# Kernel tuning notes

Measured on AMD Instinct MI355X. Metric: run time of the kernel, lower is better.

## Reference

```python
import jax, jax.numpy as jnp
import numpy as np
import math

B, S, IN, H, M = 4, 2048, 256, 128, 128  # mem_dim must equal hidden_size


def _xavier(key, shape):
    fan_in, fan_out = shape[0], shape[-1]
    lim = math.sqrt(6.0 / (fan_in + fan_out))
    return jax.random.uniform(key, shape, jnp.float32, -lim, lim)


def setup_inputs() -> dict:
    key = jax.random.key(0)
    ks = jax.random.split(key, 8)
    return dict(
        x=jax.random.normal(ks[0], (B, S, IN), jnp.float32),
        c0=jnp.zeros((M, M), jnp.float32),   # init_hidden matrix memory
        n0=jnp.zeros((M, 1), jnp.float32),   # init_hidden normalizer
        w_q=_xavier(ks[1], (IN, H)), b_q=jnp.zeros((H,), jnp.float32),
        w_k=_xavier(ks[2], (IN, M)), b_k=jnp.zeros((M,), jnp.float32),
        w_v=_xavier(ks[3], (IN, M)), b_v=jnp.zeros((M,), jnp.float32),
        w_i=_xavier(ks[4], (IN, 1)), b_i=jnp.zeros((1,), jnp.float32),
        w_f=_xavier(ks[5], (IN, 1)), b_f=jnp.zeros((1,), jnp.float32),
        w_o=_xavier(ks[6], (IN, H)), b_o=jnp.zeros((H,), jnp.float32),
    )


def reference(x, c0, n0, w_q, b_q, w_k, b_k, w_v, b_v, w_i, b_i, w_f, b_f, w_o, b_o):
    Bb, Ss, Ii = x.shape
    Mm = w_k.shape[1]
    Hh = w_q.shape[1]
    xf = x.reshape(Bb * Ss, Ii)                                  # [N, IN]
    q = xf @ w_q + b_q                                           # [N, H]
    k = (xf @ w_k + b_k) * (1.0 / math.sqrt(Mm))                 # [N, M]
    v = xf @ w_v + b_v                                           # [N, M]
    i_t = jnp.exp(xf @ w_i + b_i)                                # [N, 1]
    f_t = jax.nn.sigmoid(xf @ w_f + b_f)                         # [N, 1]
    # Original loop never updates c_prev: c_t[n] = f[n]*c0 + i[n]*outer(v[n], k[n])
    c = f_t[:, :, None] * c0[None] + i_t[:, :, None] * (v[:, :, None] * k[:, None, :])  # [N, M, M]
    n = f_t[:, :, None] * n0[None] + i_t[:, :, None] * k[:, :, None]                    # [N, M, 1]
    c = c.reshape(Bb, Ss, Mm, Mm)
    n = n.reshape(Bb, Ss, Mm, 1)
    q4 = q.reshape(Bb, Ss, Hh)
    nq = jnp.einsum('bsm,bsm->bs', n[..., 0], q4)                # n^T q
    denom = jnp.maximum(jnp.abs(nq), 1.0)[..., None]             # max(|n^T q|, 1)
    h_tilde = jnp.einsum('bsmk,bsk->bsm', c, q4) / denom         # (c_t q) / denom
    o = jax.nn.sigmoid(xf @ w_o + b_o).reshape(Bb, Ss, Hh)
    h = o * h_tilde                                              # [B, S, H]
    return (h, c, n)
```

## Files before the change

kernel.cpp:

```cpp
#include <hip/hip_runtime.h>
#include <math.h>

#define B_    4
#define S_    2048
#define IN_   256
#define H_    128
#define M_    128
#define NROWS (B_ * S_)
#define RPB   16
#define GRP   4
#define TPB   256
#define XPAD  260

typedef float f4_t __attribute__((ext_vector_type(4)));

__global__ __launch_bounds__(TPB) void xlstm_fused(
    const float* __restrict__ x,
    const float* __restrict__ c0,
    const float* __restrict__ n0,
    const float* __restrict__ w_q, const float* __restrict__ b_q,
    const float* __restrict__ w_k, const float* __restrict__ b_k,
    const float* __restrict__ w_v, const float* __restrict__ b_v,
    const float* __restrict__ w_i, const float* __restrict__ b_i,
    const float* __restrict__ w_f, const float* __restrict__ b_f,
    const float* __restrict__ w_o, const float* __restrict__ b_o,
    float* __restrict__ out_h,
    float* __restrict__ out_c,
    float* __restrict__ out_n)
{
    __shared__ float xs[RPB][XPAD];
    __shared__ float qs[RPB][M_];
    __shared__ float ks[RPB][M_];
    __shared__ float vs[RPB][M_];
    __shared__ float os_[RPB][M_];
    __shared__ float itf[RPB][2];
    __shared__ float scal[RPB][2];

    const int t    = threadIdx.x;
    const int row0 = blockIdx.x * RPB;

    for (int p4 = t; p4 < RPB * IN_ / 4; p4 += TPB) {
        int p = p4 * 4;
        float4 v = *(const float4*)(x + (size_t)row0 * IN_ + p);
        int r = p >> 8, c = p & 255;
        *(float4*)&xs[r][c] = v;
    }
    __syncthreads();

    {
        const int gr = t >> 4, gseg = t & 15;
        const float* xrow = &xs[gr][gseg * 16];
        float pi = 0.f, pf = 0.f;
        #pragma unroll
        for (int u = 0; u < 4; ++u) {
            float4 xv  = *(const float4*)(xrow + u * 4);
            float4 wiv = *(const float4*)(w_i + gseg * 16 + u * 4);
            float4 wfv = *(const float4*)(w_f + gseg * 16 + u * 4);
            pi = fmaf(xv.x, wiv.x, fmaf(xv.y, wiv.y, fmaf(xv.z, wiv.z, fmaf(xv.w, wiv.w, pi))));
            pf = fmaf(xv.x, wfv.x, fmaf(xv.y, wfv.y, fmaf(xv.z, wfv.z, fmaf(xv.w, wfv.w, pf))));
        }
        #pragma unroll
        for (int m = 1; m < 16; m <<= 1) { pi += __shfl_xor(pi, m); pf += __shfl_xor(pf, m); }
        if (gseg == 0) {
            itf[gr][0] = __expf(pi + b_i[0]);
            itf[gr][1] = 1.f / (1.f + __expf(-(pf + b_f[0])));
        }
    }

    const int cg  = t & 31;
    const int mat = (t >> 5) & 3;
    const int rh  = t >> 7;
    const int c4  = cg * 4;

    const float* W    = (mat == 0) ? w_q : (mat == 1) ? w_k : (mat == 2) ? w_v : w_o;
    const float* BIAS = (mat == 0) ? b_q : (mat == 1) ? b_k : (mat == 2) ? b_v : b_o;
    float (*DST)[M_]  = (mat == 0) ? qs  : (mat == 1) ? ks  : (mat == 2) ? vs  : os_;
    const f4_t b4 = *(const f4_t*)(BIAS + c4);
    const float kscale = 0.08838834764831843f;

    const int col = t & 127;

    #pragma unroll 1
    for (int g = 0; g < 4; ++g) {
        const int r0 = g * GRP + rh * 2;

        f4_t acc0 = (f4_t){0.f,0.f,0.f,0.f};
        f4_t acc1 = (f4_t){0.f,0.f,0.f,0.f};
        #pragma unroll 4
        for (int it = 0; it < 64; ++it) {
            const int k0 = it * 4;
            const float* wp = W + (size_t)k0 * H_ + c4;
            f4_t w0 = *(const f4_t*)(wp);
            f4_t w1 = *(const f4_t*)(wp + H_);
            f4_t w2 = *(const f4_t*)(wp + 2 * H_);
            f4_t w3 = *(const f4_t*)(wp + 3 * H_);
            f4_t xv0 = *(const f4_t*)&xs[r0][k0];
            f4_t xv1 = *(const f4_t*)&xs[r0 + 1][k0];
            acc0 += xv0.x * w0 + xv0.y * w1 + xv0.z * w2 + xv0.w * w3;
            acc1 += xv1.x * w0 + xv1.y * w1 + xv1.z * w2 + xv1.w * w3;
        }
        acc0 += b4; acc1 += b4;
        if (mat == 1) { acc0 *= kscale; acc1 *= kscale; }
        if (mat == 3) {
            acc0.x = 1.f/(1.f+__expf(-acc0.x)); acc0.y = 1.f/(1.f+__expf(-acc0.y));
            acc0.z = 1.f/(1.f+__expf(-acc0.z)); acc0.w = 1.f/(1.f+__expf(-acc0.w));
            acc1.x = 1.f/(1.f+__expf(-acc1.x)); acc1.y = 1.f/(1.f+__expf(-acc1.y));
            acc1.z = 1.f/(1.f+__expf(-acc1.z)); acc1.w = 1.f/(1.f+__expf(-acc1.w));
        }
        *(f4_t*)&DST[r0][c4]     = acc0;
        *(f4_t*)&DST[r0 + 1][c4] = acc1;
        __syncthreads();

        float c0q0 = 0.f, c0q1 = 0.f;
        {
            const float* c0row = c0 + (size_t)col * M_;
            #pragma unroll 2
            for (int j4 = 0; j4 < M_; j4 += 4) {
                f4_t w4 = *(const f4_t*)(c0row + j4);
                f4_t qa = *(const f4_t*)&qs[r0][j4];
                f4_t qb = *(const f4_t*)&qs[r0 + 1][j4];
                c0q0 = fmaf(w4.x, qa.x, fmaf(w4.y, qa.y, fmaf(w4.z, qa.z, fmaf(w4.w, qa.w, c0q0))));
                c0q1 = fmaf(w4.x, qb.x, fmaf(w4.y, qb.y, fmaf(w4.z, qb.z, fmaf(w4.w, qb.w, c0q1))));
            }
        }

        {
            const int srow = g * GRP + (t >> 6);
            const int l    = t & 63;
            float ka = ks[srow][l],      kb = ks[srow][l + 64];
            float qa = qs[srow][l],      qb = qs[srow][l + 64];
            float na = n0[l],            nb = n0[l + 64];
            float pkq = fmaf(ka, qa, kb * qb);
            float pnq = fmaf(na, qa, nb * qb);
            #pragma unroll
            for (int m = 1; m < 64; m <<= 1) { pkq += __shfl_xor(pkq, m); pnq += __shfl_xor(pnq, m); }
            if (l == 0) { scal[srow][0] = pkq; scal[srow][1] = pnq; }
        }
        __syncthreads();

        #pragma unroll
        for (int rr = 0; rr < 2; ++rr) {
            const int row = r0 + rr;
            const size_t grow = (size_t)(row0 + row);
            const float iv = itf[row][0], fv = itf[row][1];
            const float kv = ks[row][col];
            out_n[grow * M_ + col] = fmaf(fv, n0[col], iv * kv);
            const float nq    = fmaf(fv, scal[row][1], iv * scal[row][0]);
            const float denom = fmaxf(fabsf(nq), 1.0f);
            const float c0q   = rr ? c0q1 : c0q0;
            const float ht = fmaf(fv, c0q, iv * vs[row][col] * scal[row][0]) / denom;
            out_h[grow * H_ + col] = os_[row][col] * ht;
        }

        {
            const int base = t * 4;
            const int j    = base & 127;
            #pragma unroll 2
            for (int ch = 0; ch < 16; ++ch) {
                const int p = (ch << 10) + base;
                const int m = p >> 7;
                f4_t c0v = *(const f4_t*)(c0 + p);
                #pragma unroll
                for (int r = 0; r < GRP; ++r) {
                    const int row = g * GRP + r;
                    f4_t k4 = *(const f4_t*)&ks[row][j];
                    float s = itf[row][0] * vs[row][m];
                    f4_t o4 = itf[row][1] * c0v + s * k4;
                    __builtin_nontemporal_store(o4,
                        (f4_t*)(out_c + (size_t)(row0 + row) * (M_ * M_) + p));
                }
            }
        }
    }
}

extern "C" void kernel_launch(void* const* d_in, const int* in_sizes, int n_in,
                              void* d_out, int out_size, void* d_ws, size_t ws_size,
                              hipStream_t stream) {
    const float* x   = (const float*)d_in[0];
    const float* c0  = (const float*)d_in[1];
    const float* n0  = (const float*)d_in[2];
    const float* w_q = (const float*)d_in[3];  const float* b_q = (const float*)d_in[4];
    const float* w_k = (const float*)d_in[5];  const float* b_k = (const float*)d_in[6];
    const float* w_v = (const float*)d_in[7];  const float* b_v = (const float*)d_in[8];
    const float* w_i = (const float*)d_in[9];  const float* b_i = (const float*)d_in[10];
    const float* w_f = (const float*)d_in[11]; const float* b_f = (const float*)d_in[12];
    const float* w_o = (const float*)d_in[13]; const float* b_o = (const float*)d_in[14];

    float* out   = (float*)d_out;
    float* out_h = out;
    float* out_c = out + (size_t)NROWS * H_;
    float* out_n = out_c + (size_t)NROWS * M_ * M_;

    hipLaunchKernelGGL(xlstm_fused, dim3(NROWS / RPB), dim3(TPB), 0, stream,
                       x, c0, n0, w_q, b_q, w_k, b_k, w_v, b_v,
                       w_i, b_i, w_f, b_f, w_o, b_o,
                       out_h, out_c, out_n);
}
```

Baseline: 147.7 us.

## Warp-specialize fused xLSTM kernel into producer and store-consumer pipeline

Doubles the block to 512 threads and splits it by role. The first 256 threads compute the q/k/v/o projections, gates, reductions and h/n outputs for one row group. The other 256 threads stream the large c outer-product stores for the previous group, with q/k/v/o held in double-buffered shared memory. The aim is to overlap the memory-bound 8192x128x128 c writes with the projection math. In exchange, each block holds more threads and registers, which lowers occupancy, and two barriers per stage can stall whichever role runs longer.

```diff
diff --git a/kernel.cpp b/kernel.cpp
--- a/kernel.cpp
+++ b/kernel.cpp
@@ -9,12 +9,13 @@
 #define NROWS (B_ * S_)
 #define RPB   16
 #define GRP   4
-#define TPB   256
+#define NGRP  4
+#define TPB   512
 #define XPAD  260
 
 typedef float f4_t __attribute__((ext_vector_type(4)));
 
-__global__ __launch_bounds__(TPB) void xlstm_fused(
+__global__ __launch_bounds__(TPB) void xlstm_pipe(
     const float* __restrict__ x,
     const float* __restrict__ c0,
     const float* __restrict__ n0,
@@ -29,148 +30,178 @@
     float* __restrict__ out_n)
 {
     __shared__ float xs[RPB][XPAD];
-    __shared__ float qs[RPB][M_];
-    __shared__ float ks[RPB][M_];
-    __shared__ float vs[RPB][M_];
-    __shared__ float os_[RPB][M_];
+    __shared__ float bq[2][GRP][M_];
+    __shared__ float bk[2][GRP][M_];
+    __shared__ float bv[2][GRP][M_];
+    __shared__ float bo[2][GRP][M_];
     __shared__ float itf[RPB][2];
-    __shared__ float scal[RPB][2];
+    __shared__ float scalb[2][GRP][2];
 
     const int t    = threadIdx.x;
     const int row0 = blockIdx.x * RPB;
+    const bool prod = (t < 256);
 
     for (int p4 = t; p4 < RPB * IN_ / 4; p4 += TPB) {
         int p = p4 * 4;
         float4 v = *(const float4*)(x + (size_t)row0 * IN_ + p);
-        int r = p >> 8, c = p & 255;
-        *(float4*)&xs[r][c] = v;
+        *(float4*)&xs[p >> 8][p & 255] = v;
     }
     __syncthreads();
 
-    {
-        const int gr = t >> 4, gseg = t & 15;
-        const float* xrow = &xs[gr][gseg * 16];
-        float pi = 0.f, pf = 0.f;
-        #pragma unroll
-        for (int u = 0; u < 4; ++u) {
-            float4 xv  = *(const float4*)(xrow + u * 4);
-            float4 wiv = *(const float4*)(w_i + gseg * 16 + u * 4);
-            float4 wfv = *(const float4*)(w_f + gseg * 16 + u * 4);
-            pi = fmaf(xv.x, wiv.x, fmaf(xv.y, wiv.y, fmaf(xv.z, wiv.z, fmaf(xv.w, wiv.w, pi))));
-            pf = fmaf(xv.x, wfv.x, fmaf(xv.y, wfv.y, fmaf(xv.z, wfv.z, fmaf(xv.w, wfv.w, pf))));
-        }
-        #pragma unroll
-        for (int m = 1; m < 16; m <<= 1) { pi += __shfl_xor(pi, m); pf += __shfl_xor(pf, m); }
-        if (gseg == 0) {
-            itf[gr][0] = __expf(pi + b_i[0]);
-            itf[gr][1] = 1.f / (1.f + __expf(-(pf + b_f[0])));
-        }
-    }
-
     const int cg  = t & 31;
     const int mat = (t >> 5) & 3;
-    const int rh  = t >> 7;
+    const int rh  = (t >> 7) & 1;
     const int c4  = cg * 4;
-
-    const float* W    = (mat == 0) ? w_q : (mat == 1) ? w_k : (mat == 2) ? w_v : w_o;
-    const float* BIAS = (mat == 0) ? b_q : (mat == 1) ? b_k : (mat == 2) ? b_v : b_o;
-    float (*DST)[M_]  = (mat == 0) ? qs  : (mat == 1) ? ks  : (mat == 2) ? vs  : os_;
-    const f4_t b4 = *(const f4_t*)(BIAS + c4);
+    const int col = t & 127;
+    const float* W    = (mat==0)? w_q : (mat==1)? w_k : (mat==2)? w_v : w_o;
+    const float* BIAS = (mat==0)? b_q : (mat==1)? b_k : (mat==2)? b_v : b_o;
+    const f4_t bias4 = *(const f4_t*)(BIAS + c4);
     const float kscale = 0.08838834764831843f;
 
-    const int col = t & 127;
+    const int ct = t & 255;
+
+    float c0qA = 0.f, c0qB = 0.f;
 
     #pragma unroll 1
-    for (int g = 0; g < 4; ++g) {
-        const int r0 = g * GRP + rh * 2;
-
-        f4_t acc0 = (f4_t){0.f,0.f,0.f,0.f};
-        f4_t acc1 = (f4_t){0.f,0.f,0.f,0.f};
-        #pragma unroll 4
-        for (int it = 0; it < 64; ++it) {
-            const int k0 = it * 4;
-            const float* wp = W + (size_t)k0 * H_ + c4;
-            f4_t w0 = *(const f4_t*)(wp);
-            f4_t w1 = *(const f4_t*)(wp + H_);
-            f4_t w2 = *(const f4_t*)(wp + 2 * H_);
-            f4_t w3 = *(const f4_t*)(wp + 3 * H_);
-            f4_t xv0 = *(const f4_t*)&xs[r0][k0];
-            f4_t xv1 = *(const f4_t*)&xs[r0 + 1][k0];
-            acc0 += xv0.x * w0 + xv0.y * w1 + xv0.z * w2 + xv0.w * w3;
-            acc1 += xv1.x * w0 + xv1.y * w1 + xv1.z * w2 + xv1.w * w3;
-        }
-        acc0 += b4; acc1 += b4;
-        if (mat == 1) { acc0 *= kscale; acc1 *= kscale; }
-        if (mat == 3) {
-            acc0.x = 1.f/(1.f+__expf(-acc0.x)); acc0.y = 1.f/(1.f+__expf(-acc0.y));
-            acc0.z = 1.f/(1.f+__expf(-acc0.z)); acc0.w = 1.f/(1.f+__expf(-acc0.w));
-            acc1.x = 1.f/(1.f+__expf(-acc1.x)); acc1.y = 1.f/(1.f+__expf(-acc1.y));
-            acc1.z = 1.f/(1.f+__expf(-acc1.z)); acc1.w = 1.f/(1.f+__expf(-acc1.w));
-        }
-        *(f4_t*)&DST[r0][c4]     = acc0;
-        *(f4_t*)&DST[r0 + 1][c4] = acc1;
-        __syncthreads();
-
-        float c0q0 = 0.f, c0q1 = 0.f;
-        {
-            const float* c0row = c0 + (size_t)col * M_;
-            #pragma unroll 2
-            for (int j4 = 0; j4 < M_; j4 += 4) {
-                f4_t w4 = *(const f4_t*)(c0row + j4);
-                f4_t qa = *(const f4_t*)&qs[r0][j4];
-                f4_t qb = *(const f4_t*)&qs[r0 + 1][j4];
-                c0q0 = fmaf(w4.x, qa.x, fmaf(w4.y, qa.y, fmaf(w4.z, qa.z, fmaf(w4.w, qa.w, c0q0))));
-                c0q1 = fmaf(w4.x, qb.x, fmaf(w4.y, qb.y, fmaf(w4.z, qb.z, fmaf(w4.w, qb.w, c0q1))));
-            }
-        }
-
-        {
-            const int srow = g * GRP + (t >> 6);
-            const int l    = t & 63;
-            float ka = ks[srow][l],      kb = ks[srow][l + 64];
-            float qa = qs[srow][l],      qb = qs[srow][l + 64];
-            float na = n0[l],            nb = n0[l + 64];
-            float pkq = fmaf(ka, qa, kb * qb);
-            float pnq = fmaf(na, qa, nb * qb);
-            #pragma unroll
-            for (int m = 1; m < 64; m <<= 1) { pkq += __shfl_xor(pkq, m); pnq += __shfl_xor(pnq, m); }
-            if (l == 0) { scal[srow][0] = pkq; scal[srow][1] = pnq; }
-        }
-        __syncthreads();
-
-        #pragma unroll
-        for (int rr = 0; rr < 2; ++rr) {
-            const int row = r0 + rr;
-            const size_t grow = (size_t)(row0 + row);
-            const float iv = itf[row][0], fv = itf[row][1];
-            const float kv = ks[row][col];
-            out_n[grow * M_ + col] = fmaf(fv, n0[col], iv * kv);
-            const float nq    = fmaf(fv, scal[row][1], iv * scal[row][0]);
-            const float denom = fmaxf(fabsf(nq), 1.0f);
-            const float c0q   = rr ? c0q1 : c0q0;
-            const float ht = fmaf(fv, c0q, iv * vs[row][col] * scal[row][0]) / denom;
-            out_h[grow * H_ + col] = os_[row][col] * ht;
-        }
-
-        {
-            const int base = t * 4;
-            const int j    = base & 127;
+    for (int s = 0; s <= NGRP; ++s) {
+        if (prod) {
+            if (s == 0) {
+                const int gr = t >> 4, gseg = t & 15;
+                const float* xrow = &xs[gr][gseg * 16];
+                float pi = 0.f, pf = 0.f;
+                #pragma unroll
+                for (int u = 0; u < 4; ++u) {
+                    float4 xv  = *(const float4*)(xrow + u * 4);
+                    float4 wiv = *(const float4*)(w_i + gseg * 16 + u * 4);
+                    float4 wfv = *(const float4*)(w_f + gseg * 16 + u * 4);
+                    pi = fmaf(xv.x,wiv.x, fmaf(xv.y,wiv.y, fmaf(xv.z,wiv.z, fmaf(xv.w,wiv.w, pi))));
+                    pf = fmaf(xv.x,wfv.x, fmaf(xv.y,wfv.y, fmaf(xv.z,wfv.z, fmaf(xv.w,wfv.w, pf))));
+                }
+                #pragma unroll
+                for (int mm = 1; mm < 16; mm <<= 1) { pi += __shfl_xor(pi, mm); pf += __shfl_xor(pf, mm); }
+                if (gseg == 0) {
+                    itf[gr][0] = __expf(pi + b_i[0]);
+                    itf[gr][1] = 1.f / (1.f + __expf(-(pf + b_f[0])));
+                }
+            }
+            if (s > 0) {
+                const int b = (s - 1) & 1;
+                #pragma unroll
+                for (int rr = 0; rr < 2; ++rr) {
+                    const int lrow = rh * 2 + rr;
+                    const int row  = (s - 1) * GRP + lrow;
+                    const size_t grow = (size_t)(row0 + row);
+                    const float iv = itf[row][0], fv = itf[row][1];
+                    out_n[grow * M_ + col] = fmaf(fv, n0[col], iv * bk[b][lrow][col]);
+                    const float kq  = scalb[b][lrow][0];
+                    const float n0q = scalb[b][lrow][1];
+                    const float nq = fmaf(fv, n0q, iv * kq);
+                    const float denom = fmaxf(fabsf(nq), 1.f);
+                    const float c0q = rr ? c0qB : c0qA;
+                    const float ht = fmaf(fv, c0q, iv * bv[b][lrow][col] * kq) / denom;
+                    out_h[grow * H_ + col] = bo[b][lrow][col] * ht;
+                }
+            }
+            if (s < NGRP) {
+                const int b  = s & 1;
+                const int r0 = s * GRP + rh * 2;
+                f4_t acc0 = (f4_t){0.f,0.f,0.f,0.f};
+                f4_t acc1 = (f4_t){0.f,0.f,0.f,0.f};
+                #pragma unroll 4
+                for (int it = 0; it < 64; ++it) {
+                    const int k0 = it * 4;
+                    const float* wp = W + (size_t)k0 * H_ + c4;
+                    f4_t w0 = *(const f4_t*)(wp);
+                    f4_t w1 = *(const f4_t*)(wp + H_);
+                    f4_t w2 = *(const f4_t*)(wp + 2 * H_);
+                    f4_t w3 = *(const f4_t*)(wp + 3 * H_);
+                    f4_t xv0 = *(const f4_t*)&xs[r0][k0];
+                    f4_t xv1 = *(const f4_t*)&xs[r0 + 1][k0];
+                    acc0 += xv0.x*w0 + xv0.y*w1 + xv0.z*w2 + xv0.w*w3;
+                    acc1 += xv1.x*w0 + xv1.y*w1 + xv1.z*w2 + xv1.w*w3;
+                }
+                acc0 += bias4; acc1 += bias4;
+                if (mat == 1) { acc0 *= kscale; acc1 *= kscale; }
+                if (mat == 3) {
+                    acc0.x = 1.f/(1.f+__expf(-acc0.x)); acc0.y = 1.f/(1.f+__expf(-acc0.y));
+                    acc0.z = 1.f/(1.f+__expf(-acc0.z)); acc0.w = 1.f/(1.f+__expf(-acc0.w));
+                    acc1.x = 1.f/(1.f+__expf(-acc1.x)); acc1.y = 1.f/(1.f+__expf(-acc1.y));
+                    acc1.z = 1.f/(1.f+__expf(-acc1.z)); acc1.w = 1.f/(1.f+__expf(-acc1.w));
+                }
+                float (*DST)[M_] = (mat==0)? bq[b] : (mat==1)? bk[b] : (mat==2)? bv[b] : bo[b];
+                const int lr = rh * 2;
+                *(f4_t*)&DST[lr][c4]     = acc0;
+                *(f4_t*)&DST[lr + 1][c4] = acc1;
+            }
+        } else if (s > 0) {
+            const int b     = (s - 1) & 1;
+            const int gbase = (s - 1) * GRP;
+            const int base  = ct * 4;
+            const int j     = base & 127;
             #pragma unroll 2
             for (int ch = 0; ch < 16; ++ch) {
                 const int p = (ch << 10) + base;
                 const int m = p >> 7;
                 f4_t c0v = *(const f4_t*)(c0 + p);
                 #pragma unroll
-                for (int r = 0; r < GRP; ++r) {
-                    const int row = g * GRP + r;
-                    f4_t k4 = *(const f4_t*)&ks[row][j];
-                    float s = itf[row][0] * vs[row][m];
-                    f4_t o4 = itf[row][1] * c0v + s * k4;
+                for (int r = 0; r < 2; ++r) {
+                    const int row = gbase + r;
+                    f4_t k4 = *(const f4_t*)&bk[b][r][j];
+                    float sf = itf[row][0] * bv[b][r][m];
+                    f4_t o4 = itf[row][1] * c0v + sf * k4;
                     __builtin_nontemporal_store(o4,
                         (f4_t*)(out_c + (size_t)(row0 + row) * (M_ * M_) + p));
                 }
             }
         }
+        __syncthreads();
+        if (prod) {
+            if (s < NGRP) {
+                const int b  = s & 1;
+                const int lr = rh * 2;
+                float a0 = 0.f, a1 = 0.f;
+                const float* c0row = c0 + (size_t)col * M_;
+                #pragma unroll 2
+                for (int j4 = 0; j4 < M_; j4 += 4) {
+                    f4_t w4 = *(const f4_t*)(c0row + j4);
+                    f4_t qa = *(const f4_t*)&bq[b][lr][j4];
+                    f4_t qb = *(const f4_t*)&bq[b][lr + 1][j4];
+                    a0 = fmaf(w4.x,qa.x, fmaf(w4.y,qa.y, fmaf(w4.z,qa.z, fmaf(w4.w,qa.w, a0))));
+                    a1 = fmaf(w4.x,qb.x, fmaf(w4.y,qb.y, fmaf(w4.z,qb.z, fmaf(w4.w,qb.w, a1))));
+                }
+                c0qA = a0; c0qB = a1;
+                const int wv = t >> 6;
+                const int l  = t & 63;
+                const float ka  = bk[b][wv][l], kb2 = bk[b][wv][l + 64];
+                const float qa2 = bq[b][wv][l], qb2 = bq[b][wv][l + 64];
+                float pkq = fmaf(ka, qa2, kb2 * qb2);
+                float pnq = fmaf(n0[l], qa2, n0[l + 64] * qb2);
+                #pragma unroll
+                for (int mm = 1; mm < 64; mm <<= 1) { pkq += __shfl_xor(pkq, mm); pnq += __shfl_xor(pnq, mm); }
+                if (l == 0) { scalb[b][wv][0] = pkq; scalb[b][wv][1] = pnq; }
+            }
+        } else if (s > 0) {
+            const int b     = (s - 1) & 1;
+            const int gbase = (s - 1) * GRP;
+            const int base  = ct * 4;
+            const int j     = base & 127;
+            #pragma unroll 2
+            for (int ch = 0; ch < 16; ++ch) {
+                const int p = (ch << 10) + base;
+                const int m = p >> 7;
+                f4_t c0v = *(const f4_t*)(c0 + p);
+                #pragma unroll
+                for (int r = 2; r < 4; ++r) {
+                    const int row = gbase + r;
+                    f4_t k4 = *(const f4_t*)&bk[b][r][j];
+                    float sf = itf[row][0] * bv[b][r][m];
+                    f4_t o4 = itf[row][1] * c0v + sf * k4;
+                    __builtin_nontemporal_store(o4,
+                        (f4_t*)(out_c + (size_t)(row0 + row) * (M_ * M_) + p));
+                }
+            }
+        }
+        __syncthreads();
     }
 }
 
@@ -192,7 +223,7 @@
     float* out_c = out + (size_t)NROWS * H_;
     float* out_n = out_c + (size_t)NROWS * M_ * M_;
 
-    hipLaunchKernelGGL(xlstm_fused, dim3(NROWS / RPB), dim3(TPB), 0, stream,
+    hipLaunchKernelGGL(xlstm_pipe, dim3(NROWS / RPB), dim3(TPB), 0, stream,
                        x, c0, n0, w_q, b_q, w_k, b_k, w_v, b_v,
                        w_i, b_i, w_f, b_f, w_o, b_o,
                        out_h, out_c, out_n);
```

Result: faster. 138.3 us (-6.4%).
